# Performance work log

Measured on AMD Instinct MI355X. Metric: run time of the kernel, lower is better.

The kernel has to match this reference:

```python
import jax, jax.numpy as jnp
import numpy as np

N_NODES = 100000
N_EDGES = 1600000
N_GRAPHS = 2048
DIM_IN, DIM_H, DIM_FC, DIM_OUT = 128, 128, 256, 8


def _glorot(key, shape):
    fan_in, fan_out = shape[0], shape[1]
    lim = float(np.sqrt(6.0 / (fan_in + fan_out)))
    return jax.random.uniform(key, shape, jnp.float32, -lim, lim)


def setup_inputs() -> dict:
    key = jax.random.key(0)
    ks = jax.random.split(key, 16)
    x = jax.random.normal(ks[0], (N_NODES, DIM_IN), jnp.float32)
    edge_index = jax.random.randint(ks[1], (2, N_EDGES), 0, N_NODES, jnp.int64)
    batch = jnp.sort(jax.random.randint(ks[2], (N_NODES,), 0, N_GRAPHS, jnp.int64))
    inp = {"x": x, "edge_index": edge_index, "batch": batch}
    # GraphConv layers: W_rel [in,out], W_root [in,out], b [out]
    dims = [(DIM_IN, DIM_H), (DIM_H, DIM_H), (DIM_H, DIM_H), (DIM_H, DIM_H)]
    for i, (di, do) in enumerate(dims, start=1):
        inp[f"W{i}_rel"] = _glorot(ks[2 + 3 * i], (di, do))
        inp[f"W{i}_root"] = _glorot(ks[3 + 3 * i], (di, do))
        inp[f"b{i}"] = jnp.zeros((do,), jnp.float32)
    inp["fc_w"] = _glorot(ks[3], (DIM_H, DIM_FC))
    inp["fc_b"] = jnp.zeros((DIM_FC,), jnp.float32)
    inp["reg_w"] = _glorot(ks[4], (DIM_FC, DIM_OUT))
    inp["reg_b"] = jnp.zeros((DIM_OUT,), jnp.float32)
    return inp


def _graph_conv(x, src, dst, w_rel, w_root, b):
    # PyG GraphConv (aggr='add'): out_i = W_rel @ sum_{j->i} x_j + W_root @ x_i + b
    agg = jax.ops.segment_sum(x[src], dst, num_segments=N_NODES)  # [N, d_in]
    return agg @ w_rel + x @ w_root + b


def reference(x, edge_index, batch,
              W1_rel, W1_root, b1, W2_rel, W2_root, b2,
              W3_rel, W3_root, b3, W4_rel, W4_root, b4,
              fc_w, fc_b, reg_w, reg_b):
    src, dst = edge_index[0], edge_index[1]
    h = jax.nn.relu(_graph_conv(x, src, dst, W1_rel, W1_root, b1))
    h = jax.nn.relu(_graph_conv(h, src, dst, W2_rel, W2_root, b2))
    h = jax.nn.relu(_graph_conv(h, src, dst, W3_rel, W3_root, b3))
    h = jax.nn.relu(_graph_conv(h, src, dst, W4_rel, W4_root, b4))
    # global_mean_pool over graphs
    sums = jax.ops.segment_sum(h, batch, num_segments=N_GRAPHS)  # [G, d]
    cnt = jax.ops.segment_sum(jnp.ones((h.shape[0],), h.dtype), batch,
                              num_segments=N_GRAPHS)
    pooled = sums / jnp.maximum(cnt, 1.0)[:, None]
    # dropout is identity at inference
    hfc = pooled @ fc_w + fc_b
    return hfc @ reg_w + reg_b  # [G, dim_out]
```

## Files before the change

kernel.cpp:

```cpp
#include <hip/hip_runtime.h>

#define N_NODES 100000
#define N_EDGES 1600000
#define N_GRAPHS 2048
#define DIM 128

typedef short short8v __attribute__((ext_vector_type(8)));
typedef float float4v __attribute__((ext_vector_type(4)));

__device__ __forceinline__ unsigned short f2bf(float f) {
  union { float f; unsigned u; } x; x.f = f;
  unsigned r = x.u + 0x7fffu + ((x.u >> 16) & 1u);
  return (unsigned short)(r >> 16);
}
__device__ __forceinline__ float bfhi2f(unsigned bits) {
  union { unsigned u; float f; } x; x.u = bits; return x.f;
}
__device__ __forceinline__ void accum8(float* p, uint4 v) {
  p[0] += bfhi2f(v.x << 16); p[1] += bfhi2f(v.x & 0xffff0000u);
  p[2] += bfhi2f(v.y << 16); p[3] += bfhi2f(v.y & 0xffff0000u);
  p[4] += bfhi2f(v.z << 16); p[5] += bfhi2f(v.z & 0xffff0000u);
  p[6] += bfhi2f(v.w << 16); p[7] += bfhi2f(v.w & 0xffff0000u);
}

__global__ __launch_bounds__(256) void k_hist(const int* __restrict__ dst, int* __restrict__ deg,
                                              int* __restrict__ rank) {
  int i = blockIdx.x * 256 + threadIdx.x;
  if (i < N_EDGES) rank[i] = atomicAdd(&deg[dst[i]], 1);
}

__global__ __launch_bounds__(256) void k_scan1(const int* __restrict__ deg, int* __restrict__ tmp,
                                               int* __restrict__ bsum) {
  __shared__ int sh[256];
  int b = blockIdx.x, t = threadIdx.x;
  int base = b * 1024 + t * 4;
  int v[4], s = 0;
#pragma unroll
  for (int i = 0; i < 4; i++) { v[i] = (base + i < N_NODES) ? deg[base + i] : 0; s += v[i]; }
  sh[t] = s;
  __syncthreads();
  for (int off = 1; off < 256; off <<= 1) {
    int x = (t >= off) ? sh[t - off] : 0;
    __syncthreads();
    sh[t] += x;
    __syncthreads();
  }
  int run = sh[t] - s;
#pragma unroll
  for (int i = 0; i < 4; i++) { run += v[i]; if (base + i < N_NODES) tmp[base + i] = run; }
  if (t == 255) bsum[b] = sh[255];
}

__global__ void k_scan2(int* __restrict__ bsum, int nb) {
  __shared__ int sh[128];
  int t = threadIdx.x;
  int v = (t < nb) ? bsum[t] : 0;
  sh[t] = v;
  __syncthreads();
  for (int off = 1; off < 128; off <<= 1) {
    int x = (t >= off) ? sh[t - off] : 0;
    __syncthreads();
    sh[t] += x;
    __syncthreads();
  }
  if (t < nb) bsum[t] = sh[t] - v;
}

__global__ __launch_bounds__(256) void k_scan3(const int* __restrict__ tmp, const int* __restrict__ bsum,
                                               int* __restrict__ rowptr) {
  int i = blockIdx.x * 256 + threadIdx.x;
  if (i < N_NODES) rowptr[i + 1] = tmp[i] + bsum[i >> 10];
  if (i == 0) rowptr[0] = 0;
}

__global__ __launch_bounds__(256) void k_fill(const int* __restrict__ src, const int* __restrict__ dst,
                                              const int* __restrict__ rank, const int* __restrict__ rowptr,
                                              int* __restrict__ col) {
  int i = blockIdx.x * 256 + threadIdx.x;
  if (i < N_EDGES) {
    col[rowptr[dst[i]] + rank[i]] = src[i];
  }
}

__global__ __launch_bounds__(256) void k_gptr(const int* __restrict__ batch, int* __restrict__ gptr) {
  int i = blockIdx.x * 256 + threadIdx.x;
  if (i >= N_NODES) return;
  int b = batch[i];
  int a = (i == 0) ? -1 : batch[i - 1];
  for (int g = a + 1; g <= b; g++) gptr[g] = i;
  if (i == N_NODES - 1) {
    for (int g = b + 1; g <= N_GRAPHS; g++) gptr[g] = N_NODES;
  }
}

__global__ __launch_bounds__(256) void k_cvtx(const float* __restrict__ x, unsigned short* __restrict__ h) {
  int i = blockIdx.x * 256 + threadIdx.x;
  if (i < N_NODES * DIM / 4) {
    float4 v = ((const float4*)x)[i];
    unsigned lo = (unsigned)f2bf(v.x) | ((unsigned)f2bf(v.y) << 16);
    unsigned hi = (unsigned)f2bf(v.z) | ((unsigned)f2bf(v.w) << 16);
    ((uint2*)h)[i] = make_uint2(lo, hi);
  }
}

__global__ __launch_bounds__(256) void k_cvtw(const float* w0, const float* w1, const float* w2, const float* w3,
                                              const float* w4, const float* w5, const float* w6, const float* w7,
                                              unsigned short* __restrict__ wbF) {
  int i = blockIdx.x * 256 + threadIdx.x;
  if (i < 4 * 8 * 8 * 64 * 8) {
    int j = i & 7, l = (i >> 3) & 63, c = (i >> 9) & 7, kc = (i >> 12) & 7, layer = i >> 15;
    int m = layer * 2 + (kc >> 2);
    const float* w;
    switch (m) {
      case 0: w = w0; break; case 1: w = w1; break; case 2: w = w2; break; case 3: w = w3; break;
      case 4: w = w4; break; case 5: w = w5; break; case 6: w = w6; break; default: w = w7; break;
    }
    int kin = (kc & 3) * 32 + ((l >> 4) * 8) + j;
    int n = c * 16 + (l & 15);
    wbF[i] = f2bf(w[kin * 128 + n]);
  }
}

__global__ __launch_bounds__(256) void k_agg(const int* __restrict__ rowptr, const int* __restrict__ col,
                                             const unsigned short* __restrict__ hIn,
                                             unsigned short* __restrict__ aggOut) {
  int node = blockIdx.x * 4 + (threadIdx.x >> 6);
  if (node >= N_NODES) return;
  int lane = threadIdx.x & 63;
  int sub = lane >> 4;
  int li = lane & 15;
  int s0 = rowptr[node], s1 = rowptr[node + 1];
  float p[8];
#pragma unroll
  for (int j = 0; j < 8; j++) p[j] = 0.f;

  int e = s0;
  for (; e + 16 <= s1; e += 16) {
    int c0 = col[e + sub];
    int c1 = col[e + 4 + sub];
    int c2 = col[e + 8 + sub];
    int c3 = col[e + 12 + sub];
    uint4 v0 = *(const uint4*)(hIn + (size_t)c0 * DIM + li * 8);
    uint4 v1 = *(const uint4*)(hIn + (size_t)c1 * DIM + li * 8);
    uint4 v2 = *(const uint4*)(hIn + (size_t)c2 * DIM + li * 8);
    uint4 v3 = *(const uint4*)(hIn + (size_t)c3 * DIM + li * 8);
    accum8(p, v0);
    accum8(p, v1);
    accum8(p, v2);
    accum8(p, v3);
  }
  if (e + 8 <= s1) {
    int c0 = col[e + sub];
    int c1 = col[e + 4 + sub];
    uint4 v0 = *(const uint4*)(hIn + (size_t)c0 * DIM + li * 8);
    uint4 v1 = *(const uint4*)(hIn + (size_t)c1 * DIM + li * 8);
    accum8(p, v0);
    accum8(p, v1);
    e += 8;
  }
  if (e + 4 <= s1) {
    int c0 = col[e + sub];
    uint4 v0 = *(const uint4*)(hIn + (size_t)c0 * DIM + li * 8);
    accum8(p, v0);
    e += 4;
  }
  if (e + sub < s1) {
    int c0 = col[e + sub];
    uint4 v0 = *(const uint4*)(hIn + (size_t)c0 * DIM + li * 8);
    accum8(p, v0);
  }

#pragma unroll
  for (int j = 0; j < 8; j++) {
    p[j] += __shfl_xor(p[j], 16, 64);
    p[j] += __shfl_xor(p[j], 32, 64);
  }

  if (sub == 0) {
    uint4 o;
    o.x = (unsigned)f2bf(p[0]) | ((unsigned)f2bf(p[1]) << 16);
    o.y = (unsigned)f2bf(p[2]) | ((unsigned)f2bf(p[3]) << 16);
    o.z = (unsigned)f2bf(p[4]) | ((unsigned)f2bf(p[5]) << 16);
    o.w = (unsigned)f2bf(p[6]) | ((unsigned)f2bf(p[7]) << 16);
    *(uint4*)(aggOut + (size_t)node * DIM + li * 8) = o;
  }
}

__global__ __launch_bounds__(256) void k_conv(const unsigned short* __restrict__ aggB,
                                              const unsigned short* __restrict__ hIn,
                                              const unsigned short* __restrict__ wbF,
                                              const float* __restrict__ bias,
                                              unsigned short* __restrict__ hOut) {
  __shared__ uint4 As[4096];
  const int t = threadIdx.x;
  const int row0b = blockIdx.x * 128;

#pragma unroll
  for (int j = 0; j < 8; j++) {
    int r = j * 16 + (t >> 4);
    int c = t & 15;
    int rsrc = row0b + r; if (rsrc > N_NODES - 1) rsrc = N_NODES - 1;
    uint4 v = *(const uint4*)(aggB + (size_t)rsrc * DIM + c * 8);
    As[((r >> 4) * 32 + c) * 16 + ((r & 15) ^ c)] = v;
  }
#pragma unroll
  for (int j = 0; j < 8; j++) {
    int r = j * 16 + (t >> 4);
    int c = t & 15;
    int rsrc = row0b + r; if (rsrc > N_NODES - 1) rsrc = N_NODES - 1;
    uint4 v = *(const uint4*)(hIn + (size_t)rsrc * DIM + c * 8);
    As[((r >> 4) * 32 + 16 + c) * 16 + ((r & 15) ^ c)] = v;
  }
  __syncthreads();

  const int wave = t >> 6, lane = t & 63;
  const int row0 = row0b + wave * 32;

  float4v acc[2][8];
#pragma unroll
  for (int r = 0; r < 2; r++)
#pragma unroll
    for (int c = 0; c < 8; c++)
#pragma unroll
      for (int i = 0; i < 4; i++) acc[r][c][i] = 0.f;

#pragma unroll
  for (int kc = 0; kc < 8; kc++) {
    short8v afr[2];
#pragma unroll
    for (int r = 0; r < 2; r++) {
      int g = wave * 2 + r;
      int c = kc * 4 + (lane >> 4);
      int rr = (lane & 15) ^ (c & 15);
      afr[r] = *(const short8v*)&As[(g * 32 + c) * 16 + rr];
    }
#pragma unroll
    for (int c = 0; c < 8; c++) {
      short8v bfr = *(const short8v*)(wbF + (size_t)((kc * 8 + c) * 64 + lane) * 8);
#pragma unroll
      for (int r = 0; r < 2; r++)
        acc[r][c] = __builtin_amdgcn_mfma_f32_16x16x32_bf16(afr[r], bfr, acc[r][c], 0, 0, 0);
    }
  }

#pragma unroll
  for (int r = 0; r < 2; r++) {
    int rbase = row0 + r * 16 + (lane >> 4) * 4;
#pragma unroll
    for (int c = 0; c < 8; c++) {
      int colidx = c * 16 + (lane & 15);
      float bv = bias[colidx];
#pragma unroll
      for (int i = 0; i < 4; i++) {
        int row = rbase + i;
        if (row < N_NODES) {
          float v = acc[r][c][i] + bv;
          v = v > 0.f ? v : 0.f;
          hOut[row * DIM + colidx] = f2bf(v);
        }
      }
    }
  }
}

__global__ __launch_bounds__(256) void k_pool(const unsigned short* __restrict__ h,
                                              const int* __restrict__ gptr,
                                              float* __restrict__ pooledMean) {
  int g = blockIdx.x * 4 + (threadIdx.x >> 6);
  if (g >= N_GRAPHS) return;
  int lane = threadIdx.x & 63;
  int li = lane & 15;
  int s0 = gptr[g], s1 = gptr[g + 1];
  float p[8];
#pragma unroll
  for (int j = 0; j < 8; j++) p[j] = 0.f;
  int f1 = s1 * 16;
  for (int f = s0 * 16 + lane; f < f1; f += 64) {
    uint4 v = ((const uint4*)h)[f];
    accum8(p, v);
  }
#pragma unroll
  for (int j = 0; j < 8; j++) {
    p[j] += __shfl_xor(p[j], 16, 64);
    p[j] += __shfl_xor(p[j], 32, 64);
  }
  float inv = (s1 > s0) ? 1.f / (float)(s1 - s0) : 0.f;
  if (lane < 16) {
    float4 o0 = make_float4(p[0] * inv, p[1] * inv, p[2] * inv, p[3] * inv);
    float4 o1 = make_float4(p[4] * inv, p[5] * inv, p[6] * inv, p[7] * inv);
    *(float4*)(pooledMean + g * DIM + li * 8) = o0;
    *(float4*)(pooledMean + g * DIM + li * 8 + 4) = o1;
  }
}

__global__ __launch_bounds__(256) void k_fc(const float* __restrict__ pooledMean,
                                            const float* __restrict__ fc_w, const float* __restrict__ fc_b,
                                            const float* __restrict__ reg_w, const float* __restrict__ reg_b,
                                            float* __restrict__ out) {
  __shared__ float sp[128];
  __shared__ float shfc[256];
  __shared__ float red[64];
  int g = blockIdx.x, t = threadIdx.x;
  if (t < 128) sp[t] = pooledMean[g * DIM + t];
  __syncthreads();
  float a = fc_b[t];
  for (int k = 0; k < 128; k++) a += sp[k] * fc_w[k * 256 + t];
  shfc[t] = a;
  __syncthreads();
  if (t < 64) {
    int o = t & 7, seg = t >> 3;
    float r = 0.f;
    for (int j = seg * 32; j < seg * 32 + 32; j++) r += shfc[j] * reg_w[j * 8 + o];
    red[t] = r;
  }
  __syncthreads();
  if (t < 8) {
    float r = reg_b[t];
    for (int s = 0; s < 8; s++) r += red[s * 8 + t];
    out[g * 8 + t] = r;
  }
}

extern "C" void kernel_launch(void* const* d_in, const int* in_sizes, int n_in,
                              void* d_out, int out_size, void* d_ws, size_t ws_size,
                              hipStream_t stream) {
  (void)in_sizes; (void)n_in; (void)out_size; (void)ws_size;
  const float* x = (const float*)d_in[0];
  const int* ei = (const int*)d_in[1];
  const int* src = ei;
  const int* dst = ei + N_EDGES;
  const int* batch = (const int*)d_in[2];
  const float* Wrel[4]  = {(const float*)d_in[3], (const float*)d_in[6], (const float*)d_in[9],  (const float*)d_in[12]};
  const float* Wroot[4] = {(const float*)d_in[4], (const float*)d_in[7], (const float*)d_in[10], (const float*)d_in[13]};
  const float* bias[4]  = {(const float*)d_in[5], (const float*)d_in[8], (const float*)d_in[11], (const float*)d_in[14]};
  const float* fc_w  = (const float*)d_in[15];
  const float* fc_b  = (const float*)d_in[16];
  const float* reg_w = (const float*)d_in[17];
  const float* reg_b = (const float*)d_in[18];
  float* out = (float*)d_out;

  char* ws = (char*)d_ws;
  size_t off = 0;
  auto alloc = [&](size_t b) -> char* {
    char* p = ws + off;
    off = (off + b + 255) & ~(size_t)255;
    return p;
  };
  int* rowptr = (int*)alloc((N_NODES + 1) * 4);
  int* deg    = (int*)alloc(N_NODES * 4);
  int* tmp    = (int*)alloc(N_NODES * 4);
  int* bsum   = (int*)alloc(128 * 4);
  int* rank   = (int*)alloc((size_t)N_EDGES * 4);
  int* colws  = (int*)alloc((size_t)N_EDGES * 4);
  int* gptr   = (int*)alloc((N_GRAPHS + 1) * 4);
  unsigned short* wbF = (unsigned short*)alloc((size_t)4 * 32768 * 2);
  unsigned short* h_a = (unsigned short*)alloc((size_t)N_NODES * DIM * 2);
  unsigned short* h_b = (unsigned short*)alloc((size_t)N_NODES * DIM * 2);
  unsigned short* agg = (unsigned short*)alloc((size_t)N_NODES * DIM * 2);
  float* pooled = (float*)alloc((size_t)N_GRAPHS * DIM * 4);

  hipMemsetAsync(deg, 0, N_NODES * 4, stream);

  const int EB = (N_EDGES + 255) / 256;
  const int NB1 = (N_NODES + 1023) / 1024;

  k_hist<<<EB, 256, 0, stream>>>(dst, deg, rank);
  k_scan1<<<NB1, 256, 0, stream>>>(deg, tmp, bsum);
  k_scan2<<<1, 128, 0, stream>>>(bsum, NB1);
  k_scan3<<<(N_NODES + 255) / 256, 256, 0, stream>>>(tmp, bsum, rowptr);
  k_fill<<<EB, 256, 0, stream>>>(src, dst, rank, rowptr, colws);
  k_gptr<<<(N_NODES + 255) / 256, 256, 0, stream>>>(batch, gptr);

  k_cvtx<<<(N_NODES * DIM / 4 + 255) / 256, 256, 0, stream>>>(x, h_a);
  k_cvtw<<<(4 * 32768 + 255) / 256, 256, 0, stream>>>(
      Wrel[0], Wroot[0], Wrel[1], Wroot[1], Wrel[2], Wroot[2], Wrel[3], Wroot[3], wbF);

  unsigned short* h_in = h_a;
  unsigned short* h_out = h_b;
  for (int l = 0; l < 4; l++) {
    k_agg<<<(N_NODES + 3) / 4, 256, 0, stream>>>(rowptr, colws, h_in, agg);
    k_conv<<<(N_NODES + 127) / 128, 256, 0, stream>>>(
        agg, h_in, wbF + (size_t)l * 32768, bias[l], h_out);
    unsigned short* t2 = h_in; h_in = h_out; h_out = t2;
  }

  k_pool<<<(N_GRAPHS + 3) / 4, 256, 0, stream>>>(h_in, gptr, pooled);
  k_fc<<<N_GRAPHS, 256, 0, stream>>>(pooled, fc_w, fc_b, reg_w, reg_b, out);
}
```

Baseline: 628.6 us.

## Build CSR via two-level bucket sort with shared-memory atomics

Replaces the global-atomic degree histogram and rank-based scatter with a two-pass bucket sort. Edges are first bucketed by dst>>9 using per-block shared-memory counters and a scanned count matrix, then each bucket block builds rowptr and col with local shared atomics. This is meant to remove 1.6M global atomics and the random scatter writes into col. In exchange it adds an extra pass over edges through an 8-byte packed buffer, and the finish stage runs only 196 blocks, which limits parallelism. Neighbor order within a row may also change.

```diff
diff --git a/kernel.cpp b/kernel.cpp
--- a/kernel.cpp
+++ b/kernel.cpp
@@ -4,6 +4,12 @@
 #define N_EDGES 1600000
 #define N_GRAPHS 2048
 #define DIM 128
+
+#define NBUK 196
+#define BUKSH 9
+#define NCH 256
+#define EPB 6250
+#define NMAT (NBUK * NCH)
 
 typedef short short8v __attribute__((ext_vector_type(8)));
 typedef float float4v __attribute__((ext_vector_type(4)));
@@ -23,20 +29,25 @@
   p[6] += bfhi2f(v.w << 16); p[7] += bfhi2f(v.w & 0xffff0000u);
 }
 
-__global__ __launch_bounds__(256) void k_hist(const int* __restrict__ dst, int* __restrict__ deg,
-                                              int* __restrict__ rank) {
-  int i = blockIdx.x * 256 + threadIdx.x;
-  if (i < N_EDGES) rank[i] = atomicAdd(&deg[dst[i]], 1);
-}
-
-__global__ __launch_bounds__(256) void k_scan1(const int* __restrict__ deg, int* __restrict__ tmp,
-                                               int* __restrict__ bsum) {
+__global__ __launch_bounds__(256) void k_bcount(const int* __restrict__ dst, int* __restrict__ cntmat) {
+  __shared__ int cnt[NBUK];
+  int b = blockIdx.x, t = threadIdx.x;
+  if (t < NBUK) cnt[t] = 0;
+  __syncthreads();
+  int e0 = b * EPB;
+  for (int j = t; j < EPB; j += 256) atomicAdd(&cnt[dst[e0 + j] >> BUKSH], 1);
+  __syncthreads();
+  if (t < NBUK) cntmat[t * NCH + b] = cnt[t];
+}
+
+__global__ __launch_bounds__(256) void k_scan1g(const int* __restrict__ in, int n,
+                                                int* __restrict__ tmp, int* __restrict__ bsum) {
   __shared__ int sh[256];
   int b = blockIdx.x, t = threadIdx.x;
   int base = b * 1024 + t * 4;
   int v[4], s = 0;
 #pragma unroll
-  for (int i = 0; i < 4; i++) { v[i] = (base + i < N_NODES) ? deg[base + i] : 0; s += v[i]; }
+  for (int i = 0; i < 4; i++) { v[i] = (base + i < n) ? in[base + i] : 0; s += v[i]; }
   sh[t] = s;
   __syncthreads();
   for (int off = 1; off < 256; off <<= 1) {
@@ -47,11 +58,11 @@
   }
   int run = sh[t] - s;
 #pragma unroll
-  for (int i = 0; i < 4; i++) { run += v[i]; if (base + i < N_NODES) tmp[base + i] = run; }
+  for (int i = 0; i < 4; i++) { run += v[i]; if (base + i < n) tmp[base + i] = run; }
   if (t == 255) bsum[b] = sh[255];
 }
 
-__global__ void k_scan2(int* __restrict__ bsum, int nb) {
+__global__ void k_scan2g(int* __restrict__ bsum, int nb) {
   __shared__ int sh[128];
   int t = threadIdx.x;
   int v = (t < nb) ? bsum[t] : 0;
@@ -66,19 +77,61 @@
   if (t < nb) bsum[t] = sh[t] - v;
 }
 
-__global__ __launch_bounds__(256) void k_scan3(const int* __restrict__ tmp, const int* __restrict__ bsum,
-                                               int* __restrict__ rowptr) {
+__global__ __launch_bounds__(256) void k_exc(const int* __restrict__ tmp, const int* __restrict__ bsum,
+                                             const int* __restrict__ in, int n, int* __restrict__ outExc) {
   int i = blockIdx.x * 256 + threadIdx.x;
-  if (i < N_NODES) rowptr[i + 1] = tmp[i] + bsum[i >> 10];
-  if (i == 0) rowptr[0] = 0;
-}
-
-__global__ __launch_bounds__(256) void k_fill(const int* __restrict__ src, const int* __restrict__ dst,
-                                              const int* __restrict__ rank, const int* __restrict__ rowptr,
-                                              int* __restrict__ col) {
-  int i = blockIdx.x * 256 + threadIdx.x;
-  if (i < N_EDGES) {
-    col[rowptr[dst[i]] + rank[i]] = src[i];
+  if (i < n) outExc[i] = tmp[i] + bsum[i >> 10] - in[i];
+}
+
+__global__ __launch_bounds__(256) void k_bscatter(const int* __restrict__ src, const int* __restrict__ dst,
+                                                  const int* __restrict__ base, int2* __restrict__ epk) {
+  __shared__ int cur[NBUK];
+  int b = blockIdx.x, t = threadIdx.x;
+  if (t < NBUK) cur[t] = base[t * NCH + b];
+  __syncthreads();
+  int e0 = b * EPB;
+  for (int j = t; j < EPB; j += 256) {
+    int s = src[e0 + j], d = dst[e0 + j];
+    int pos = atomicAdd(&cur[d >> BUKSH], 1);
+    epk[pos] = make_int2(s, d);
+  }
+}
+
+__global__ __launch_bounds__(256) void k_bfinish(const int2* __restrict__ epk, const int* __restrict__ base,
+                                                 int* __restrict__ rowptr, int* __restrict__ col) {
+  __shared__ int a[512];
+  __shared__ int sh[256];
+  int k = blockIdx.x, t = threadIdx.x;
+  int bstart = base[k * NCH];
+  int bend = (k + 1 < NBUK) ? base[(k + 1) * NCH] : N_EDGES;
+  a[t] = 0; a[t + 256] = 0;
+  __syncthreads();
+  for (int i = bstart + t; i < bend; i += 256) atomicAdd(&a[epk[i].y - (k << BUKSH)], 1);
+  __syncthreads();
+  int c0 = a[2 * t], c1 = a[2 * t + 1];
+  int s = c0 + c1;
+  sh[t] = s;
+  __syncthreads();
+  for (int off = 1; off < 256; off <<= 1) {
+    int x = (t >= off) ? sh[t - off] : 0;
+    __syncthreads();
+    sh[t] += x;
+    __syncthreads();
+  }
+  int excl = sh[t] - s;
+  int st0 = bstart + excl;
+  int st1 = st0 + c0;
+  int g0 = (k << BUKSH) + 2 * t, g1 = g0 + 1;
+  if (g0 < N_NODES) rowptr[g0] = st0;
+  if (g1 < N_NODES) rowptr[g1] = st1;
+  if (k == NBUK - 1 && t == 0) rowptr[N_NODES] = N_EDGES;
+  __syncthreads();
+  a[2 * t] = st0; a[2 * t + 1] = st1;
+  __syncthreads();
+  for (int i = bstart + t; i < bend; i += 256) {
+    int2 e = epk[i];
+    int pos = atomicAdd(&a[e.y - (k << BUKSH)], 1);
+    col[pos] = e.x;
   }
 }
 
@@ -347,10 +400,11 @@
     return p;
   };
   int* rowptr = (int*)alloc((N_NODES + 1) * 4);
-  int* deg    = (int*)alloc(N_NODES * 4);
-  int* tmp    = (int*)alloc(N_NODES * 4);
-  int* bsum   = (int*)alloc(128 * 4);
-  int* rank   = (int*)alloc((size_t)N_EDGES * 4);
+  int* cntmat = (int*)alloc((size_t)NMAT * 4);
+  int* tmpB   = (int*)alloc((size_t)NMAT * 4);
+  int* bsumB  = (int*)alloc(64 * 4);
+  int* base   = (int*)alloc((size_t)NMAT * 4);
+  int2* epk   = (int2*)alloc((size_t)N_EDGES * 8);
   int* colws  = (int*)alloc((size_t)N_EDGES * 4);
   int* gptr   = (int*)alloc((N_GRAPHS + 1) * 4);
   unsigned short* wbF = (unsigned short*)alloc((size_t)4 * 32768 * 2);
@@ -359,18 +413,14 @@
   unsigned short* agg = (unsigned short*)alloc((size_t)N_NODES * DIM * 2);
   float* pooled = (float*)alloc((size_t)N_GRAPHS * DIM * 4);
 
-  hipMemsetAsync(deg, 0, N_NODES * 4, stream);
-
-  const int EB = (N_EDGES + 255) / 256;
-  const int NB1 = (N_NODES + 1023) / 1024;
-
-  k_hist<<<EB, 256, 0, stream>>>(dst, deg, rank);
-  k_scan1<<<NB1, 256, 0, stream>>>(deg, tmp, bsum);
-  k_scan2<<<1, 128, 0, stream>>>(bsum, NB1);
-  k_scan3<<<(N_NODES + 255) / 256, 256, 0, stream>>>(tmp, bsum, rowptr);
-  k_fill<<<EB, 256, 0, stream>>>(src, dst, rank, rowptr, colws);
+  k_bcount<<<NCH, 256, 0, stream>>>(dst, cntmat);
+  k_scan1g<<<NMAT / 1024, 256, 0, stream>>>(cntmat, NMAT, tmpB, bsumB);
+  k_scan2g<<<1, 128, 0, stream>>>(bsumB, NMAT / 1024);
+  k_exc<<<(NMAT + 255) / 256, 256, 0, stream>>>(tmpB, bsumB, cntmat, NMAT, base);
+  k_bscatter<<<NCH, 256, 0, stream>>>(src, dst, base, epk);
+  k_bfinish<<<NBUK, 256, 0, stream>>>(epk, base, rowptr, colws);
+
   k_gptr<<<(N_NODES + 255) / 256, 256, 0, stream>>>(batch, gptr);
-
   k_cvtx<<<(N_NODES * DIM / 4 + 255) / 256, 256, 0, stream>>>(x, h_a);
   k_cvtw<<<(4 * 32768 + 255) / 256, 256, 0, stream>>>(
       Wrel[0], Wroot[0], Wrel[1], Wroot[1], Wrel[2], Wroot[2], Wrel[3], Wroot[3], wbF);
```

New measurement: 583.3 us. -7.2%, faster.
